# Kernel optimization log

Hardware: AMD Instinct MI355X
Metric: run time of the kernel (lower is better)

Reference implementation:

```python
import jax, jax.numpy as jnp
import numpy as np

N_NODES = 100000
N_EDGES = 1600000
D_IN = 64
D_OUT = 64


def setup_inputs() -> dict:
    key = jax.random.key(0)
    k1, k2, k3, k4, k5 = jax.random.split(key, 5)
    x = jax.random.normal(k1, (N_NODES, D_IN), dtype=jnp.float32)
    edge_src = jax.random.randint(k2, (N_EDGES,), 0, N_NODES, dtype=jnp.int32)
    edge_dst = jax.random.randint(k3, (N_EDGES,), 0, N_NODES, dtype=jnp.int32)
    edge_val = jnp.ones((N_EDGES,), dtype=jnp.float32)
    stdv = 1.0 / np.sqrt(D_OUT)
    weight = jax.random.uniform(k4, (D_IN, D_OUT), minval=-stdv, maxval=stdv, dtype=jnp.float32)
    epsilon = jnp.ones((1,), dtype=jnp.float32)
    bias = jax.random.uniform(k5, (D_OUT,), minval=-stdv, maxval=stdv, dtype=jnp.float32)
    return {"x": x, "edge_src": edge_src, "edge_dst": edge_dst,
            "edge_val": edge_val, "weight": weight, "epsilon": epsilon, "bias": bias}


def reference(x, edge_src, edge_dst, edge_val, weight, epsilon, bias):
    # spmm(adj, x): row i of adj gathers neighbors -> segment_sum over edge_src
    # adj[i, j] = edge_val for edge (src=i, dst=j)
    msgs = edge_val[:, None] * x[edge_dst]            # [E, D_in]
    agg = jax.ops.segment_sum(msgs, edge_src, num_segments=N_NODES)  # [N, D_in]
    # epsilon * eye(N) @ x == epsilon * x (avoid O(N^2) identity)
    rep = agg + epsilon * x                            # [N, D_in]
    out = rep @ weight + bias                          # [N, D_out]
    return out, rep
```

## Files before the change

kernel.cpp:

```cpp
#include <hip/hip_runtime.h>

#define N_NODES 100000
#define N_EDGES 1600000
#define D 64

#define NB 391
#define BLKA 196
#define EPB 8192
#define NT (NB * BLKA)
#define NCH 75

#define WS_GHIST   0
#define WS_PART    76672
#define WS_ROWPTR  76800
#define WS_KEYS    176832
#define WS_PAIRS   1776832

__global__ __launch_bounds__(256) void k_bucket_hist(
    const int* __restrict__ esrc, int* __restrict__ ghist)
{
    __shared__ int h[NB];
    int t = threadIdx.x;
    for (int j = t; j < NB; j += 256) h[j] = 0;
    __syncthreads();
    int base = blockIdx.x * EPB;
    #pragma unroll
    for (int i = 0; i < 8; ++i) {
        int e0 = base + i * 1024 + t * 4;
        if (e0 < N_EDGES) {
            int4 s4 = *(const int4*)(esrc + e0);
            atomicAdd(&h[s4.x >> 8], 1);
            atomicAdd(&h[s4.y >> 8], 1);
            atomicAdd(&h[s4.z >> 8], 1);
            atomicAdd(&h[s4.w >> 8], 1);
        }
    }
    __syncthreads();
    for (int j = t; j < NB; j += 256) ghist[j * BLKA + blockIdx.x] = h[j];
}

__global__ __launch_bounds__(1024) void k_ghist_scan1(
    const int* __restrict__ ghist, int* __restrict__ partial)
{
    __shared__ int sred[16];
    int t = threadIdx.x;
    int idx = blockIdx.x * 1024 + t;
    int v = (idx < NT) ? ghist[idx] : 0;
    #pragma unroll
    for (int off = 32; off; off >>= 1) v += __shfl_down(v, off, 64);
    if ((t & 63) == 0) sred[t >> 6] = v;
    __syncthreads();
    if (t < 16) {
        int w = sred[t];
        #pragma unroll
        for (int off = 8; off; off >>= 1) w += __shfl_down(w, off, 16);
        if (t == 0) partial[blockIdx.x] = w;
    }
}

__global__ __launch_bounds__(1024) void k_ghist_scan2(
    int* __restrict__ ghist, const int* __restrict__ partial)
{
    __shared__ int red1[16];
    __shared__ int wsum[16];
    __shared__ int bc;
    int t = threadIdx.x;
    int lane = t & 63, wid = t >> 6;

    int pv = (t < NCH) ? partial[t] : 0;
    int a1 = (t < (int)blockIdx.x) ? pv : 0;
    #pragma unroll
    for (int off = 32; off; off >>= 1) a1 += __shfl_down(a1, off, 64);
    if (lane == 0) red1[wid] = a1;
    __syncthreads();
    if (t < 16) {
        int w = red1[t];
        #pragma unroll
        for (int off = 8; off; off >>= 1) w += __shfl_down(w, off, 16);
        if (t == 0) bc = w;
    }
    __syncthreads();

    int idx = blockIdx.x * 1024 + t;
    int v = (idx < NT) ? ghist[idx] : 0;
    int s = v;
    #pragma unroll
    for (int off = 1; off < 64; off <<= 1) {
        int y = __shfl_up(s, off, 64);
        if (lane >= off) s += y;
    }
    if (lane == 63) wsum[wid] = s;
    __syncthreads();
    if (t < 16) {
        int w = wsum[t];
        #pragma unroll
        for (int off = 1; off < 16; off <<= 1) {
            int y = __shfl_up(w, off, 16);
            if (t >= off) w += y;
        }
        wsum[t] = w;
    }
    __syncthreads();
    int prefix = wid ? wsum[wid - 1] : 0;
    if (idx < NT) ghist[idx] = bc + prefix + s - v;
}

__global__ __launch_bounds__(256) void k_scatter(
    const int* __restrict__ esrc, const int* __restrict__ edst,
    const float* __restrict__ eval_, const int* __restrict__ ghist,
    int* __restrict__ keys, int2* __restrict__ tpairs)
{
    __shared__ int base[NB];
    int t = threadIdx.x;
    for (int j = t; j < NB; j += 256) base[j] = ghist[j * BLKA + blockIdx.x];
    __syncthreads();
    int eb = blockIdx.x * EPB;
    #pragma unroll
    for (int i = 0; i < 8; ++i) {
        int e0 = eb + i * 1024 + t * 4;
        if (e0 < N_EDGES) {
            int4 s4 = *(const int4*)(esrc + e0);
            int4 d4 = *(const int4*)(edst + e0);
            float4 v4 = *(const float4*)(eval_ + e0);
            int p0 = atomicAdd(&base[s4.x >> 8], 1);
            int p1 = atomicAdd(&base[s4.y >> 8], 1);
            int p2 = atomicAdd(&base[s4.z >> 8], 1);
            int p3 = atomicAdd(&base[s4.w >> 8], 1);
            keys[p0] = s4.x; tpairs[p0] = make_int2(d4.x, __float_as_int(v4.x));
            keys[p1] = s4.y; tpairs[p1] = make_int2(d4.y, __float_as_int(v4.y));
            keys[p2] = s4.z; tpairs[p2] = make_int2(d4.z, __float_as_int(v4.z));
            keys[p3] = s4.w; tpairs[p3] = make_int2(d4.w, __float_as_int(v4.w));
        }
    }
}

__global__ __launch_bounds__(256) void k_build_csr(
    const int* __restrict__ keys, const int2* __restrict__ tpairs,
    const int* __restrict__ ghist, int* __restrict__ row_ptr,
    int2* __restrict__ pairs)
{
    __shared__ int hist[256], cursor[256], wsum4[4];
    int b = blockIdx.x, t = threadIdx.x;
    int s_begin = ghist[b * BLKA];
    int s_end = (b + 1 < NB) ? ghist[(b + 1) * BLKA] : N_EDGES;
    hist[t] = 0;
    __syncthreads();
    #pragma unroll 4
    for (int pos = s_begin + t; pos < s_end; pos += 256)
        atomicAdd(&hist[keys[pos] & 255], 1);
    __syncthreads();
    int lane = t & 63, wid = t >> 6;
    int v = hist[t], s = v;
    #pragma unroll
    for (int off = 1; off < 64; off <<= 1) {
        int y = __shfl_up(s, off, 64);
        if (lane >= off) s += y;
    }
    if (lane == 63) wsum4[wid] = s;
    __syncthreads();
    if (t == 0) {
        int r = 0;
        #pragma unroll
        for (int k = 0; k < 4; ++k) { int x = wsum4[k]; wsum4[k] = r; r += x; }
    }
    __syncthreads();
    int excl = wsum4[wid] + s - v;
    cursor[t] = excl;
    int node = (b << 8) + t;
    if (node <= N_NODES) row_ptr[node] = s_begin + excl;
    __syncthreads();
    #pragma unroll 4
    for (int pos = s_begin + t; pos < s_end; pos += 256) {
        int k = keys[pos] & 255;
        int2 pv = tpairs[pos];
        int p = atomicAdd(&cursor[k], 1);
        pairs[s_begin + p] = pv;
    }
}

#define GATHER_BLOCKS 2048

__global__ __launch_bounds__(256) void k_gather(
    const float* __restrict__ x, const int* __restrict__ row_ptr,
    const int2* __restrict__ pairs, const float* __restrict__ epsilon,
    float* __restrict__ rep)
{
    int w = (blockIdx.x * 256 + threadIdx.x) >> 6;
    int nw = gridDim.x * 4;
    int lane = threadIdx.x & 63;
    int sub = lane >> 4;
    int f4 = lane & 15;
    float eps = epsilon[0];
    const float4* x4 = (const float4*)x;

    int r0 = (int)((long long)w * N_NODES / nw);
    int r1 = (int)((long long)(w + 1) * N_NODES / nw);

    for (int row = r0; row < r1; ++row) {
        int start = __builtin_amdgcn_readfirstlane(row_ptr[row]);
        int end   = __builtin_amdgcn_readfirstlane(row_ptr[row + 1]);
        float4 acc = make_float4(0.f, 0.f, 0.f, 0.f);
        for (int j = start; j < end; j += 16) {
            int2 p[4];
            #pragma unroll
            for (int u = 0; u < 4; ++u) {
                int e = j + u * 4 + sub;
                p[u] = (e < end) ? pairs[e] : make_int2(0, 0);
            }
            float4 a[4];
            #pragma unroll
            for (int u = 0; u < 4; ++u)
                a[u] = x4[(size_t)p[u].x * 16 + f4];
            #pragma unroll
            for (int u = 0; u < 4; ++u) {
                float vv = __int_as_float(p[u].y);
                acc.x += vv * a[u].x; acc.y += vv * a[u].y;
                acc.z += vv * a[u].z; acc.w += vv * a[u].w;
            }
        }
        #pragma unroll
        for (int off = 16; off <= 32; off <<= 1) {
            acc.x += __shfl_xor(acc.x, off, 64);
            acc.y += __shfl_xor(acc.y, off, 64);
            acc.z += __shfl_xor(acc.z, off, 64);
            acc.w += __shfl_xor(acc.w, off, 64);
        }
        if (sub == 0) {
            float4 xv = x4[(size_t)row * 16 + f4];
            float4 o = make_float4(acc.x + eps * xv.x, acc.y + eps * xv.y,
                                   acc.z + eps * xv.z, acc.w + eps * xv.w);
            ((float4*)rep)[(size_t)row * 16 + f4] = o;
        }
    }
}

#define GEMM_TM 64
__global__ __launch_bounds__(256) void k_gemm(
    const float* __restrict__ rep, const float* __restrict__ weight,
    const float* __restrict__ bias, float* __restrict__ out)
{
    __shared__ float rep_s[GEMM_TM * 68];
    __shared__ float Ws[D * D];
    int t = threadIdx.x;
    {
        const float4* w4 = (const float4*)weight;
        float4* s4 = (float4*)Ws;
        #pragma unroll
        for (int i = 0; i < (D * D / 4) / 256; ++i)
            s4[t + i * 256] = w4[t + i * 256];
    }
    int row0 = blockIdx.x * GEMM_TM;
    {
        const float4* r4 = (const float4*)rep;
        #pragma unroll
        for (int i = 0; i < 4; ++i) {
            int f = t + i * 256;
            int rr = f >> 4, kk4 = f & 15;
            float4 v = (row0 + rr < N_NODES) ? r4[(size_t)(row0 + rr) * 16 + kk4]
                                             : make_float4(0.f, 0.f, 0.f, 0.f);
            rep_s[rr * 68 + kk4 * 4 + 0] = v.x;
            rep_s[rr * 68 + kk4 * 4 + 1] = v.y;
            rep_s[rr * 68 + kk4 * 4 + 2] = v.z;
            rep_s[rr * 68 + kk4 * 4 + 3] = v.w;
        }
    }
    __syncthreads();

    int tx = t & 15, ty = t >> 4;
    float4 b4 = ((const float4*)bias)[tx];
    float acc[4][4];
    #pragma unroll
    for (int i = 0; i < 4; ++i) {
        acc[i][0] = b4.x; acc[i][1] = b4.y; acc[i][2] = b4.z; acc[i][3] = b4.w;
    }
    #pragma unroll 4
    for (int k4 = 0; k4 < 16; ++k4) {
        float4 rv[4];
        #pragma unroll
        for (int i = 0; i < 4; ++i)
            rv[i] = *(const float4*)&rep_s[(ty * 4 + i) * 68 + k4 * 4];
        #pragma unroll
        for (int kk = 0; kk < 4; ++kk) {
            float4 wv = *(const float4*)&Ws[(k4 * 4 + kk) * D + tx * 4];
            #pragma unroll
            for (int i = 0; i < 4; ++i) {
                float r = ((const float*)&rv[i])[kk];
                acc[i][0] += r * wv.x;
                acc[i][1] += r * wv.y;
                acc[i][2] += r * wv.z;
                acc[i][3] += r * wv.w;
            }
        }
    }
    #pragma unroll
    for (int i = 0; i < 4; ++i) {
        int row = row0 + ty * 4 + i;
        if (row < N_NODES)
            *(float4*)&out[(size_t)row * D + tx * 4] =
                make_float4(acc[i][0], acc[i][1], acc[i][2], acc[i][3]);
    }
}

extern "C" void kernel_launch(void* const* d_in, const int* in_sizes, int n_in,
                              void* d_out, int out_size, void* d_ws, size_t ws_size,
                              hipStream_t stream) {
    const float* x    = (const float*)d_in[0];
    const int*   esrc = (const int*)  d_in[1];
    const int*   edst = (const int*)  d_in[2];
    const float* ev   = (const float*)d_in[3];
    const float* w    = (const float*)d_in[4];
    const float* eps  = (const float*)d_in[5];
    const float* bias = (const float*)d_in[6];

    float* out = (float*)d_out;
    float* rep = out + (size_t)N_NODES * D;

    int* ws      = (int*)d_ws;
    int* ghist   = ws + WS_GHIST;
    int* partial = ws + WS_PART;
    int* row_ptr = ws + WS_ROWPTR;
    int* keys    = ws + WS_KEYS;
    int2* pairs  = (int2*)(ws + WS_PAIRS);
    int2* tpairs = (int2*)rep;

    k_bucket_hist<<<BLKA, 256, 0, stream>>>(esrc, ghist);
    k_ghist_scan1<<<NCH, 1024, 0, stream>>>(ghist, partial);
    k_ghist_scan2<<<NCH, 1024, 0, stream>>>(ghist, partial);
    k_scatter<<<BLKA, 256, 0, stream>>>(esrc, edst, ev, ghist, keys, tpairs);
    k_build_csr<<<NB, 256, 0, stream>>>(keys, tpairs, ghist, row_ptr, pairs);
    k_gather<<<GATHER_BLOCKS, 256, 0, stream>>>(x, row_ptr, pairs, eps, rep);
    k_gemm<<<(N_NODES + GEMM_TM - 1) / GEMM_TM, 256, 0, stream>>>(rep, w, bias, out);
}
```

Before: 236.5 us.

## Replace full CSR build with 64-node bucket sort and shared-memory atomic accumulation

Buckets edges by 64-node tiles instead of 256-node buckets, drops the second-level CSR build kernel, and packs the local row index into the pair's high bits. A new per-tile gather kernel accumulates messages into a shared-memory tile with LDS float atomics, using rotated columns to spread bank conflicts, then adds eps*x and writes rep. This removes one full pass over the edge list and the keys array, at the cost of LDS atomic contention, scalar 4-byte x loads instead of float4, and a larger bucket histogram and scan.

```diff
diff --git a/kernel.cpp b/kernel.cpp
--- a/kernel.cpp
+++ b/kernel.cpp
@@ -4,24 +4,23 @@
 #define N_EDGES 1600000
 #define D 64
 
-#define NB 391
+#define TILE_N 64
+#define NBUK 1563
 #define BLKA 196
 #define EPB 8192
-#define NT (NB * BLKA)
-#define NCH 75
+#define NT (NBUK * BLKA)
+#define NCH 300
 
 #define WS_GHIST   0
-#define WS_PART    76672
-#define WS_ROWPTR  76800
-#define WS_KEYS    176832
-#define WS_PAIRS   1776832
+#define WS_PART    306432
+#define WS_TPAIRS  306816
 
 __global__ __launch_bounds__(256) void k_bucket_hist(
     const int* __restrict__ esrc, int* __restrict__ ghist)
 {
-    __shared__ int h[NB];
-    int t = threadIdx.x;
-    for (int j = t; j < NB; j += 256) h[j] = 0;
+    __shared__ int h[NBUK];
+    int t = threadIdx.x;
+    for (int j = t; j < NBUK; j += 256) h[j] = 0;
     __syncthreads();
     int base = blockIdx.x * EPB;
     #pragma unroll
@@ -29,14 +28,14 @@
         int e0 = base + i * 1024 + t * 4;
         if (e0 < N_EDGES) {
             int4 s4 = *(const int4*)(esrc + e0);
-            atomicAdd(&h[s4.x >> 8], 1);
-            atomicAdd(&h[s4.y >> 8], 1);
-            atomicAdd(&h[s4.z >> 8], 1);
-            atomicAdd(&h[s4.w >> 8], 1);
-        }
-    }
-    __syncthreads();
-    for (int j = t; j < NB; j += 256) ghist[j * BLKA + blockIdx.x] = h[j];
+            atomicAdd(&h[s4.x >> 6], 1);
+            atomicAdd(&h[s4.y >> 6], 1);
+            atomicAdd(&h[s4.z >> 6], 1);
+            atomicAdd(&h[s4.w >> 6], 1);
+        }
+    }
+    __syncthreads();
+    for (int j = t; j < NBUK; j += 256) ghist[j * BLKA + blockIdx.x] = h[j];
 }
 
 __global__ __launch_bounds__(1024) void k_ghist_scan1(
@@ -108,11 +107,11 @@
 __global__ __launch_bounds__(256) void k_scatter(
     const int* __restrict__ esrc, const int* __restrict__ edst,
     const float* __restrict__ eval_, const int* __restrict__ ghist,
-    int* __restrict__ keys, int2* __restrict__ tpairs)
-{
-    __shared__ int base[NB];
-    int t = threadIdx.x;
-    for (int j = t; j < NB; j += 256) base[j] = ghist[j * BLKA + blockIdx.x];
+    int2* __restrict__ tpairs)
+{
+    __shared__ int base[NBUK];
+    int t = threadIdx.x;
+    for (int j = t; j < NBUK; j += 256) base[j] = ghist[j * BLKA + blockIdx.x];
     __syncthreads();
     int eb = blockIdx.x * EPB;
     #pragma unroll
@@ -122,114 +121,84 @@
             int4 s4 = *(const int4*)(esrc + e0);
             int4 d4 = *(const int4*)(edst + e0);
             float4 v4 = *(const float4*)(eval_ + e0);
-            int p0 = atomicAdd(&base[s4.x >> 8], 1);
-            int p1 = atomicAdd(&base[s4.y >> 8], 1);
-            int p2 = atomicAdd(&base[s4.z >> 8], 1);
-            int p3 = atomicAdd(&base[s4.w >> 8], 1);
-            keys[p0] = s4.x; tpairs[p0] = make_int2(d4.x, __float_as_int(v4.x));
-            keys[p1] = s4.y; tpairs[p1] = make_int2(d4.y, __float_as_int(v4.y));
-            keys[p2] = s4.z; tpairs[p2] = make_int2(d4.z, __float_as_int(v4.z));
-            keys[p3] = s4.w; tpairs[p3] = make_int2(d4.w, __float_as_int(v4.w));
-        }
-    }
-}
-
-__global__ __launch_bounds__(256) void k_build_csr(
-    const int* __restrict__ keys, const int2* __restrict__ tpairs,
-    const int* __restrict__ ghist, int* __restrict__ row_ptr,
-    int2* __restrict__ pairs)
-{
-    __shared__ int hist[256], cursor[256], wsum4[4];
+            int p0 = atomicAdd(&base[s4.x >> 6], 1);
+            int p1 = atomicAdd(&base[s4.y >> 6], 1);
+            int p2 = atomicAdd(&base[s4.z >> 6], 1);
+            int p3 = atomicAdd(&base[s4.w >> 6], 1);
+            tpairs[p0] = make_int2(((s4.x & 63) << 17) | d4.x, __float_as_int(v4.x));
+            tpairs[p1] = make_int2(((s4.y & 63) << 17) | d4.y, __float_as_int(v4.y));
+            tpairs[p2] = make_int2(((s4.z & 63) << 17) | d4.z, __float_as_int(v4.z));
+            tpairs[p3] = make_int2(((s4.w & 63) << 17) | d4.w, __float_as_int(v4.w));
+        }
+    }
+}
+
+__global__ __launch_bounds__(256) void k_tile_gather(
+    const float* __restrict__ x, const int2* __restrict__ tpairs,
+    const int* __restrict__ ghist, const float* __restrict__ epsilon,
+    float* __restrict__ rep)
+{
+    __shared__ float tile[TILE_N * D];
     int b = blockIdx.x, t = threadIdx.x;
-    int s_begin = ghist[b * BLKA];
-    int s_end = (b + 1 < NB) ? ghist[(b + 1) * BLKA] : N_EDGES;
-    hist[t] = 0;
-    __syncthreads();
-    #pragma unroll 4
-    for (int pos = s_begin + t; pos < s_end; pos += 256)
-        atomicAdd(&hist[keys[pos] & 255], 1);
-    __syncthreads();
-    int lane = t & 63, wid = t >> 6;
-    int v = hist[t], s = v;
-    #pragma unroll
-    for (int off = 1; off < 64; off <<= 1) {
-        int y = __shfl_up(s, off, 64);
-        if (lane >= off) s += y;
-    }
-    if (lane == 63) wsum4[wid] = s;
-    __syncthreads();
-    if (t == 0) {
-        int r = 0;
-        #pragma unroll
-        for (int k = 0; k < 4; ++k) { int x = wsum4[k]; wsum4[k] = r; r += x; }
-    }
-    __syncthreads();
-    int excl = wsum4[wid] + s - v;
-    cursor[t] = excl;
-    int node = (b << 8) + t;
-    if (node <= N_NODES) row_ptr[node] = s_begin + excl;
-    __syncthreads();
-    #pragma unroll 4
-    for (int pos = s_begin + t; pos < s_end; pos += 256) {
-        int k = keys[pos] & 255;
-        int2 pv = tpairs[pos];
-        int p = atomicAdd(&cursor[k], 1);
-        pairs[s_begin + p] = pv;
-    }
-}
-
-#define GATHER_BLOCKS 2048
-
-__global__ __launch_bounds__(256) void k_gather(
-    const float* __restrict__ x, const int* __restrict__ row_ptr,
-    const int2* __restrict__ pairs, const float* __restrict__ epsilon,
-    float* __restrict__ rep)
-{
-    int w = (blockIdx.x * 256 + threadIdx.x) >> 6;
-    int nw = gridDim.x * 4;
-    int lane = threadIdx.x & 63;
-    int sub = lane >> 4;
-    int f4 = lane & 15;
+    {
+        float4* t4 = (float4*)tile;
+        #pragma unroll
+        for (int i = 0; i < 4; ++i)
+            t4[t + i * 256] = make_float4(0.f, 0.f, 0.f, 0.f);
+    }
+    __syncthreads();
+
+    int begin = ghist[b * BLKA];
+    int end   = (b + 1 < NBUK) ? ghist[(b + 1) * BLKA] : N_EDGES;
+
+    int wv = t >> 6, lane = t & 63;
+    int sub = lane >> 4, f4 = lane & 15;
+
+    for (int j = begin + wv * 16; j < end; j += 4 * 16) {
+        int2 p[4];
+        #pragma unroll
+        for (int u = 0; u < 4; ++u) {
+            int e = j + u * 4 + sub;
+            p[u] = (e < end) ? tpairs[e] : make_int2(0, 0);
+        }
+        float a[4][4];
+        #pragma unroll
+        for (int u = 0; u < 4; ++u) {
+            int dst = p[u].x & 0x1FFFF;
+            #pragma unroll
+            for (int c = 0; c < 4; ++c)
+                a[u][c] = x[dst * D + f4 + 16 * c];
+        }
+        #pragma unroll
+        for (int u = 0; u < 4; ++u) {
+            float vv = __int_as_float(p[u].y);
+            int n = p[u].x >> 17;
+            #pragma unroll
+            for (int c = 0; c < 4; ++c) {
+                int col = (f4 + 16 * c + n) & 63;
+                atomicAdd(&tile[n * D + col], vv * a[u][c]);
+            }
+        }
+    }
+    __syncthreads();
+
     float eps = epsilon[0];
+    int n0 = b * TILE_N;
     const float4* x4 = (const float4*)x;
-
-    int r0 = (int)((long long)w * N_NODES / nw);
-    int r1 = (int)((long long)(w + 1) * N_NODES / nw);
-
-    for (int row = r0; row < r1; ++row) {
-        int start = __builtin_amdgcn_readfirstlane(row_ptr[row]);
-        int end   = __builtin_amdgcn_readfirstlane(row_ptr[row + 1]);
-        float4 acc = make_float4(0.f, 0.f, 0.f, 0.f);
-        for (int j = start; j < end; j += 16) {
-            int2 p[4];
-            #pragma unroll
-            for (int u = 0; u < 4; ++u) {
-                int e = j + u * 4 + sub;
-                p[u] = (e < end) ? pairs[e] : make_int2(0, 0);
-            }
-            float4 a[4];
-            #pragma unroll
-            for (int u = 0; u < 4; ++u)
-                a[u] = x4[(size_t)p[u].x * 16 + f4];
-            #pragma unroll
-            for (int u = 0; u < 4; ++u) {
-                float vv = __int_as_float(p[u].y);
-                acc.x += vv * a[u].x; acc.y += vv * a[u].y;
-                acc.z += vv * a[u].z; acc.w += vv * a[u].w;
-            }
-        }
-        #pragma unroll
-        for (int off = 16; off <= 32; off <<= 1) {
-            acc.x += __shfl_xor(acc.x, off, 64);
-            acc.y += __shfl_xor(acc.y, off, 64);
-            acc.z += __shfl_xor(acc.z, off, 64);
-            acc.w += __shfl_xor(acc.w, off, 64);
-        }
-        if (sub == 0) {
-            float4 xv = x4[(size_t)row * 16 + f4];
-            float4 o = make_float4(acc.x + eps * xv.x, acc.y + eps * xv.y,
-                                   acc.z + eps * xv.z, acc.w + eps * xv.w);
-            ((float4*)rep)[(size_t)row * 16 + f4] = o;
+    #pragma unroll
+    for (int i = 0; i < 4; ++i) {
+        int f = t + i * 256;
+        int n = f >> 4, c4 = f & 15;
+        int node = n0 + n;
+        if (node < N_NODES) {
+            float r0 = tile[n * D + ((c4 * 4 + 0 + n) & 63)];
+            float r1 = tile[n * D + ((c4 * 4 + 1 + n) & 63)];
+            float r2 = tile[n * D + ((c4 * 4 + 2 + n) & 63)];
+            float r3 = tile[n * D + ((c4 * 4 + 3 + n) & 63)];
+            float4 xv = x4[(size_t)node * 16 + c4];
+            ((float4*)rep)[(size_t)node * 16 + c4] =
+                make_float4(r0 + eps * xv.x, r1 + eps * xv.y,
+                            r2 + eps * xv.z, r3 + eps * xv.w);
         }
     }
 }
@@ -318,16 +287,12 @@
     int* ws      = (int*)d_ws;
     int* ghist   = ws + WS_GHIST;
     int* partial = ws + WS_PART;
-    int* row_ptr = ws + WS_ROWPTR;
-    int* keys    = ws + WS_KEYS;
-    int2* pairs  = (int2*)(ws + WS_PAIRS);
-    int2* tpairs = (int2*)rep;
+    int2* tpairs = (int2*)(ws + WS_TPAIRS);
 
     k_bucket_hist<<<BLKA, 256, 0, stream>>>(esrc, ghist);
     k_ghist_scan1<<<NCH, 1024, 0, stream>>>(ghist, partial);
     k_ghist_scan2<<<NCH, 1024, 0, stream>>>(ghist, partial);
-    k_scatter<<<BLKA, 256, 0, stream>>>(esrc, edst, ev, ghist, keys, tpairs);
-    k_build_csr<<<NB, 256, 0, stream>>>(keys, tpairs, ghist, row_ptr, pairs);
-    k_gather<<<GATHER_BLOCKS, 256, 0, stream>>>(x, row_ptr, pairs, eps, rep);
+    k_scatter<<<BLKA, 256, 0, stream>>>(esrc, edst, ev, ghist, tpairs);
+    k_tile_gather<<<NBUK, 256, 0, stream>>>(x, tpairs, ghist, eps, rep);
     k_gemm<<<(N_NODES + GEMM_TM - 1) / GEMM_TM, 256, 0, stream>>>(rep, w, bias, out);
 }
```

New measurement: 739.3 us. +212.6%, slower.

## Pack low source bits into pair word, drop keys array, use finer buckets

Applied to the files above, without the earlier changes.

The separate keys array is removed. The low 7 bits of each source node are packed into the upper bits of the destination index inside the pair (dst fits in 17 bits), and the gather masks them off. Buckets shrink from 256 to 128 nodes and blocks shrink to 2048 edges, giving 782 buckets and 782 histogram blocks. This cuts a 1.6M-element write and read. In exchange the global histogram grows to about 611K entries and the scan gets more blocks.

```diff
diff --git a/kernel.cpp b/kernel.cpp
--- a/kernel.cpp
+++ b/kernel.cpp
@@ -4,19 +4,18 @@
 #define N_EDGES 1600000
 #define D 64
 
-#define NB 391
-#define BLKA 196
-#define EPB 8192
+#define NB 782
+#define BLKA 782
+#define EPB 2048
 #define NT (NB * BLKA)
-#define NCH 75
+#define NCH 598
 
 #define WS_GHIST   0
-#define WS_PART    76672
-#define WS_ROWPTR  76800
-#define WS_KEYS    176832
-#define WS_PAIRS   1776832
-
-__global__ __launch_bounds__(256) void k_bucket_hist(
+#define WS_PART    611584
+#define WS_ROWPTR  612224
+#define WS_PAIRS   712256
+
+__global__ __launch_bounds__(256) void k_hist(
     const int* __restrict__ esrc, int* __restrict__ ghist)
 {
     __shared__ int h[NB];
@@ -25,21 +24,21 @@
     __syncthreads();
     int base = blockIdx.x * EPB;
     #pragma unroll
-    for (int i = 0; i < 8; ++i) {
+    for (int i = 0; i < 2; ++i) {
         int e0 = base + i * 1024 + t * 4;
         if (e0 < N_EDGES) {
             int4 s4 = *(const int4*)(esrc + e0);
-            atomicAdd(&h[s4.x >> 8], 1);
-            atomicAdd(&h[s4.y >> 8], 1);
-            atomicAdd(&h[s4.z >> 8], 1);
-            atomicAdd(&h[s4.w >> 8], 1);
+            atomicAdd(&h[s4.x >> 7], 1);
+            atomicAdd(&h[s4.y >> 7], 1);
+            atomicAdd(&h[s4.z >> 7], 1);
+            atomicAdd(&h[s4.w >> 7], 1);
         }
     }
     __syncthreads();
     for (int j = t; j < NB; j += 256) ghist[j * BLKA + blockIdx.x] = h[j];
 }
 
-__global__ __launch_bounds__(1024) void k_ghist_scan1(
+__global__ __launch_bounds__(1024) void k_scan1(
     const int* __restrict__ ghist, int* __restrict__ partial)
 {
     __shared__ int sred[16];
@@ -58,7 +57,7 @@
     }
 }
 
-__global__ __launch_bounds__(1024) void k_ghist_scan2(
+__global__ __launch_bounds__(1024) void k_scan2(
     int* __restrict__ ghist, const int* __restrict__ partial)
 {
     __shared__ int red1[16];
@@ -108,7 +107,7 @@
 __global__ __launch_bounds__(256) void k_scatter(
     const int* __restrict__ esrc, const int* __restrict__ edst,
     const float* __restrict__ eval_, const int* __restrict__ ghist,
-    int* __restrict__ keys, int2* __restrict__ tpairs)
+    int2* __restrict__ tpairs)
 {
     __shared__ int base[NB];
     int t = threadIdx.x;
@@ -116,63 +115,63 @@
     __syncthreads();
     int eb = blockIdx.x * EPB;
     #pragma unroll
-    for (int i = 0; i < 8; ++i) {
+    for (int i = 0; i < 2; ++i) {
         int e0 = eb + i * 1024 + t * 4;
         if (e0 < N_EDGES) {
             int4 s4 = *(const int4*)(esrc + e0);
             int4 d4 = *(const int4*)(edst + e0);
             float4 v4 = *(const float4*)(eval_ + e0);
-            int p0 = atomicAdd(&base[s4.x >> 8], 1);
-            int p1 = atomicAdd(&base[s4.y >> 8], 1);
-            int p2 = atomicAdd(&base[s4.z >> 8], 1);
-            int p3 = atomicAdd(&base[s4.w >> 8], 1);
-            keys[p0] = s4.x; tpairs[p0] = make_int2(d4.x, __float_as_int(v4.x));
-            keys[p1] = s4.y; tpairs[p1] = make_int2(d4.y, __float_as_int(v4.y));
-            keys[p2] = s4.z; tpairs[p2] = make_int2(d4.z, __float_as_int(v4.z));
-            keys[p3] = s4.w; tpairs[p3] = make_int2(d4.w, __float_as_int(v4.w));
-        }
-    }
-}
-
-__global__ __launch_bounds__(256) void k_build_csr(
-    const int* __restrict__ keys, const int2* __restrict__ tpairs,
-    const int* __restrict__ ghist, int* __restrict__ row_ptr,
-    int2* __restrict__ pairs)
-{
-    __shared__ int hist[256], cursor[256], wsum4[4];
+            int p0 = atomicAdd(&base[s4.x >> 7], 1);
+            int p1 = atomicAdd(&base[s4.y >> 7], 1);
+            int p2 = atomicAdd(&base[s4.z >> 7], 1);
+            int p3 = atomicAdd(&base[s4.w >> 7], 1);
+            tpairs[p0] = make_int2(((s4.x & 127) << 17) | d4.x, __float_as_int(v4.x));
+            tpairs[p1] = make_int2(((s4.y & 127) << 17) | d4.y, __float_as_int(v4.y));
+            tpairs[p2] = make_int2(((s4.z & 127) << 17) | d4.z, __float_as_int(v4.z));
+            tpairs[p3] = make_int2(((s4.w & 127) << 17) | d4.w, __float_as_int(v4.w));
+        }
+    }
+}
+
+__global__ __launch_bounds__(256) void k_build(
+    const int2* __restrict__ tpairs, const int* __restrict__ ghist,
+    int* __restrict__ row_ptr, int2* __restrict__ pairs)
+{
+    __shared__ int hist[128], cursor[128], wsum2[2];
     int b = blockIdx.x, t = threadIdx.x;
     int s_begin = ghist[b * BLKA];
     int s_end = (b + 1 < NB) ? ghist[(b + 1) * BLKA] : N_EDGES;
-    hist[t] = 0;
+    if (t < 128) hist[t] = 0;
     __syncthreads();
     #pragma unroll 4
     for (int pos = s_begin + t; pos < s_end; pos += 256)
-        atomicAdd(&hist[keys[pos] & 255], 1);
+        atomicAdd(&hist[(tpairs[pos].x >> 17) & 127], 1);
     __syncthreads();
     int lane = t & 63, wid = t >> 6;
-    int v = hist[t], s = v;
-    #pragma unroll
-    for (int off = 1; off < 64; off <<= 1) {
-        int y = __shfl_up(s, off, 64);
-        if (lane >= off) s += y;
-    }
-    if (lane == 63) wsum4[wid] = s;
-    __syncthreads();
-    if (t == 0) {
-        int r = 0;
-        #pragma unroll
-        for (int k = 0; k < 4; ++k) { int x = wsum4[k]; wsum4[k] = r; r += x; }
-    }
-    __syncthreads();
-    int excl = wsum4[wid] + s - v;
-    cursor[t] = excl;
-    int node = (b << 8) + t;
-    if (node <= N_NODES) row_ptr[node] = s_begin + excl;
+    int v = 0, s = 0;
+    if (t < 128) {
+        v = hist[t]; s = v;
+        #pragma unroll
+        for (int off = 1; off < 64; off <<= 1) {
+            int y = __shfl_up(s, off, 64);
+            if (lane >= off) s += y;
+        }
+        if (lane == 63) wsum2[wid] = s;
+    }
+    __syncthreads();
+    if (t == 0) { int x0 = wsum2[0]; wsum2[0] = 0; wsum2[1] = x0; }
+    __syncthreads();
+    if (t < 128) {
+        int excl = wsum2[wid] + s - v;
+        cursor[t] = excl;
+        int node = (b << 7) + t;
+        if (node <= N_NODES) row_ptr[node] = s_begin + excl;
+    }
     __syncthreads();
     #pragma unroll 4
     for (int pos = s_begin + t; pos < s_end; pos += 256) {
-        int k = keys[pos] & 255;
         int2 pv = tpairs[pos];
+        int k = (pv.x >> 17) & 127;
         int p = atomicAdd(&cursor[k], 1);
         pairs[s_begin + p] = pv;
     }
@@ -210,7 +209,7 @@
             float4 a[4];
             #pragma unroll
             for (int u = 0; u < 4; ++u)
-                a[u] = x4[(size_t)p[u].x * 16 + f4];
+                a[u] = x4[(size_t)(p[u].x & 0x1FFFF) * 16 + f4];
             #pragma unroll
             for (int u = 0; u < 4; ++u) {
                 float vv = __int_as_float(p[u].y);
@@ -319,15 +318,14 @@
     int* ghist   = ws + WS_GHIST;
     int* partial = ws + WS_PART;
     int* row_ptr = ws + WS_ROWPTR;
-    int* keys    = ws + WS_KEYS;
     int2* pairs  = (int2*)(ws + WS_PAIRS);
     int2* tpairs = (int2*)rep;
 
-    k_bucket_hist<<<BLKA, 256, 0, stream>>>(esrc, ghist);
-    k_ghist_scan1<<<NCH, 1024, 0, stream>>>(ghist, partial);
-    k_ghist_scan2<<<NCH, 1024, 0, stream>>>(ghist, partial);
-    k_scatter<<<BLKA, 256, 0, stream>>>(esrc, edst, ev, ghist, keys, tpairs);
-    k_build_csr<<<NB, 256, 0, stream>>>(keys, tpairs, ghist, row_ptr, pairs);
+    k_hist<<<BLKA, 256, 0, stream>>>(esrc, ghist);
+    k_scan1<<<NCH, 1024, 0, stream>>>(ghist, partial);
+    k_scan2<<<NCH, 1024, 0, stream>>>(ghist, partial);
+    k_scatter<<<BLKA, 256, 0, stream>>>(esrc, edst, ev, ghist, tpairs);
+    k_build<<<NB, 256, 0, stream>>>(tpairs, ghist, row_ptr, pairs);
     k_gather<<<GATHER_BLOCKS, 256, 0, stream>>>(x, row_ptr, pairs, eps, rep);
     k_gemm<<<(N_NODES + GEMM_TM - 1) / GEMM_TM, 256, 0, stream>>>(rep, w, bias, out);
 }
```

After: 222.5 us. -5.9%, faster.

## Gather from fp16 copy of x and pack edges into 32-bit words

Applied to the files above, without the earlier changes.

Converts x to fp16 in the histogram kernel and has the gather read half-precision rows, which halves the random-gather traffic. The separate keys array is dropped by packing the low source bits into the destination field. CSR entries shrink to 32 bits: 17 bits of destination plus a 15-bit truncated half of the edge value. The cost is precision loss in both x and the edge weights (the value drops its lowest mantissa bit), which could break tolerance for general inputs. The bucketing grid is also doubled to 391 blocks of 4096 edges.

```diff
diff --git a/kernel.cpp b/kernel.cpp
--- a/kernel.cpp
+++ b/kernel.cpp
@@ -1,23 +1,25 @@
 #include <hip/hip_runtime.h>
+#include <hip/hip_fp16.h>
 
 #define N_NODES 100000
 #define N_EDGES 1600000
 #define D 64
 
 #define NB 391
-#define BLKA 196
-#define EPB 8192
+#define BLKA 391
+#define EPB 4096
 #define NT (NB * BLKA)
-#define NCH 75
+#define NCH 150
 
 #define WS_GHIST   0
-#define WS_PART    76672
-#define WS_ROWPTR  76800
-#define WS_KEYS    176832
-#define WS_PAIRS   1776832
-
-__global__ __launch_bounds__(256) void k_bucket_hist(
-    const int* __restrict__ esrc, int* __restrict__ ghist)
+#define WS_PART    152896
+#define WS_ROWPTR  153152
+#define WS_PAIRSU  253184
+#define WS_XH      1853184
+
+__global__ __launch_bounds__(256) void k_hist_cvt(
+    const int* __restrict__ esrc, const float* __restrict__ x,
+    int* __restrict__ ghist, uint2* __restrict__ xh2)
 {
     __shared__ int h[NB];
     int t = threadIdx.x;
@@ -25,7 +27,7 @@
     __syncthreads();
     int base = blockIdx.x * EPB;
     #pragma unroll
-    for (int i = 0; i < 8; ++i) {
+    for (int i = 0; i < 4; ++i) {
         int e0 = base + i * 1024 + t * 4;
         if (e0 < N_EDGES) {
             int4 s4 = *(const int4*)(esrc + e0);
@@ -35,11 +37,27 @@
             atomicAdd(&h[s4.w >> 8], 1);
         }
     }
+    {
+        const float4* x4 = (const float4*)x;
+        #pragma unroll
+        for (int i = 0; i < 16; ++i) {
+            int f = blockIdx.x * 4096 + i * 256 + t;
+            if (f < N_NODES * (D / 4)) {
+                float4 v = x4[f];
+                uint2 o;
+                o.x = (uint)__half_as_ushort(__float2half_rn(v.x)) |
+                      ((uint)__half_as_ushort(__float2half_rn(v.y)) << 16);
+                o.y = (uint)__half_as_ushort(__float2half_rn(v.z)) |
+                      ((uint)__half_as_ushort(__float2half_rn(v.w)) << 16);
+                xh2[f] = o;
+            }
+        }
+    }
     __syncthreads();
     for (int j = t; j < NB; j += 256) ghist[j * BLKA + blockIdx.x] = h[j];
 }
 
-__global__ __launch_bounds__(1024) void k_ghist_scan1(
+__global__ __launch_bounds__(1024) void k_scan1(
     const int* __restrict__ ghist, int* __restrict__ partial)
 {
     __shared__ int sred[16];
@@ -58,7 +76,7 @@
     }
 }
 
-__global__ __launch_bounds__(1024) void k_ghist_scan2(
+__global__ __launch_bounds__(1024) void k_scan2(
     int* __restrict__ ghist, const int* __restrict__ partial)
 {
     __shared__ int red1[16];
@@ -108,7 +126,7 @@
 __global__ __launch_bounds__(256) void k_scatter(
     const int* __restrict__ esrc, const int* __restrict__ edst,
     const float* __restrict__ eval_, const int* __restrict__ ghist,
-    int* __restrict__ keys, int2* __restrict__ tpairs)
+    int2* __restrict__ tpairs)
 {
     __shared__ int base[NB];
     int t = threadIdx.x;
@@ -116,7 +134,7 @@
     __syncthreads();
     int eb = blockIdx.x * EPB;
     #pragma unroll
-    for (int i = 0; i < 8; ++i) {
+    for (int i = 0; i < 4; ++i) {
         int e0 = eb + i * 1024 + t * 4;
         if (e0 < N_EDGES) {
             int4 s4 = *(const int4*)(esrc + e0);
@@ -126,18 +144,17 @@
             int p1 = atomicAdd(&base[s4.y >> 8], 1);
             int p2 = atomicAdd(&base[s4.z >> 8], 1);
             int p3 = atomicAdd(&base[s4.w >> 8], 1);
-            keys[p0] = s4.x; tpairs[p0] = make_int2(d4.x, __float_as_int(v4.x));
-            keys[p1] = s4.y; tpairs[p1] = make_int2(d4.y, __float_as_int(v4.y));
-            keys[p2] = s4.z; tpairs[p2] = make_int2(d4.z, __float_as_int(v4.z));
-            keys[p3] = s4.w; tpairs[p3] = make_int2(d4.w, __float_as_int(v4.w));
-        }
-    }
-}
-
-__global__ __launch_bounds__(256) void k_build_csr(
-    const int* __restrict__ keys, const int2* __restrict__ tpairs,
-    const int* __restrict__ ghist, int* __restrict__ row_ptr,
-    int2* __restrict__ pairs)
+            tpairs[p0] = make_int2(((s4.x & 255) << 17) | d4.x, __float_as_int(v4.x));
+            tpairs[p1] = make_int2(((s4.y & 255) << 17) | d4.y, __float_as_int(v4.y));
+            tpairs[p2] = make_int2(((s4.z & 255) << 17) | d4.z, __float_as_int(v4.z));
+            tpairs[p3] = make_int2(((s4.w & 255) << 17) | d4.w, __float_as_int(v4.w));
+        }
+    }
+}
+
+__global__ __launch_bounds__(256) void k_build(
+    const int2* __restrict__ tpairs, const int* __restrict__ ghist,
+    int* __restrict__ row_ptr, unsigned int* __restrict__ pairsu)
 {
     __shared__ int hist[256], cursor[256], wsum4[4];
     int b = blockIdx.x, t = threadIdx.x;
@@ -147,7 +164,7 @@
     __syncthreads();
     #pragma unroll 4
     for (int pos = s_begin + t; pos < s_end; pos += 256)
-        atomicAdd(&hist[keys[pos] & 255], 1);
+        atomicAdd(&hist[(tpairs[pos].x >> 17) & 255], 1);
     __syncthreads();
     int lane = t & 63, wid = t >> 6;
     int v = hist[t], s = v;
@@ -161,7 +178,7 @@
     if (t == 0) {
         int r = 0;
         #pragma unroll
-        for (int k = 0; k < 4; ++k) { int x = wsum4[k]; wsum4[k] = r; r += x; }
+        for (int k = 0; k < 4; ++k) { int w = wsum4[k]; wsum4[k] = r; r += w; }
     }
     __syncthreads();
     int excl = wsum4[wid] + s - v;
@@ -171,19 +188,22 @@
     __syncthreads();
     #pragma unroll 4
     for (int pos = s_begin + t; pos < s_end; pos += 256) {
-        int k = keys[pos] & 255;
         int2 pv = tpairs[pos];
+        int k = (pv.x >> 17) & 255;
         int p = atomicAdd(&cursor[k], 1);
-        pairs[s_begin + p] = pv;
+        unsigned int dst = (unsigned int)pv.x & 0x1FFFFu;
+        unsigned int hb = (unsigned int)__half_as_ushort(
+            __float2half_rn(__int_as_float(pv.y)));
+        pairsu[s_begin + p] = (dst << 15) | (hb >> 1);
     }
 }
 
 #define GATHER_BLOCKS 2048
 
 __global__ __launch_bounds__(256) void k_gather(
-    const float* __restrict__ x, const int* __restrict__ row_ptr,
-    const int2* __restrict__ pairs, const float* __restrict__ epsilon,
-    float* __restrict__ rep)
+    const float* __restrict__ x, const uint2* __restrict__ xh2,
+    const int* __restrict__ row_ptr, const unsigned int* __restrict__ pairsu,
+    const float* __restrict__ epsilon, float* __restrict__ rep)
 {
     int w = (blockIdx.x * 256 + threadIdx.x) >> 6;
     int nw = gridDim.x * 4;
@@ -201,21 +221,24 @@
         int end   = __builtin_amdgcn_readfirstlane(row_ptr[row + 1]);
         float4 acc = make_float4(0.f, 0.f, 0.f, 0.f);
         for (int j = start; j < end; j += 16) {
-            int2 p[4];
+            unsigned int pk[4];
             #pragma unroll
             for (int u = 0; u < 4; ++u) {
                 int e = j + u * 4 + sub;
-                p[u] = (e < end) ? pairs[e] : make_int2(0, 0);
+                pk[u] = (e < end) ? pairsu[e] : 0u;
             }
-            float4 a[4];
+            uint2 a[4];
             #pragma unroll
             for (int u = 0; u < 4; ++u)
-                a[u] = x4[(size_t)p[u].x * 16 + f4];
+                a[u] = xh2[(size_t)(pk[u] >> 15) * 16 + f4];
             #pragma unroll
             for (int u = 0; u < 4; ++u) {
-                float vv = __int_as_float(p[u].y);
-                acc.x += vv * a[u].x; acc.y += vv * a[u].y;
-                acc.z += vv * a[u].z; acc.w += vv * a[u].w;
+                unsigned short hb = (unsigned short)((pk[u] & 0x7FFFu) << 1);
+                float vv = __half2float(__ushort_as_half(hb));
+                float2 f01 = __half22float2(*reinterpret_cast<const __half2*>(&a[u].x));
+                float2 f23 = __half22float2(*reinterpret_cast<const __half2*>(&a[u].y));
+                acc.x += vv * f01.x; acc.y += vv * f01.y;
+                acc.z += vv * f23.x; acc.w += vv * f23.y;
             }
         }
         #pragma unroll
@@ -315,19 +338,19 @@
     float* out = (float*)d_out;
     float* rep = out + (size_t)N_NODES * D;
 
-    int* ws      = (int*)d_ws;
-    int* ghist   = ws + WS_GHIST;
-    int* partial = ws + WS_PART;
-    int* row_ptr = ws + WS_ROWPTR;
-    int* keys    = ws + WS_KEYS;
-    int2* pairs  = (int2*)(ws + WS_PAIRS);
-    int2* tpairs = (int2*)rep;
-
-    k_bucket_hist<<<BLKA, 256, 0, stream>>>(esrc, ghist);
-    k_ghist_scan1<<<NCH, 1024, 0, stream>>>(ghist, partial);
-    k_ghist_scan2<<<NCH, 1024, 0, stream>>>(ghist, partial);
-    k_scatter<<<BLKA, 256, 0, stream>>>(esrc, edst, ev, ghist, keys, tpairs);
-    k_build_csr<<<NB, 256, 0, stream>>>(keys, tpairs, ghist, row_ptr, pairs);
-    k_gather<<<GATHER_BLOCKS, 256, 0, stream>>>(x, row_ptr, pairs, eps, rep);
+    int* ws       = (int*)d_ws;
+    int* ghist    = ws + WS_GHIST;
+    int* partial  = ws + WS_PART;
+    int* row_ptr  = ws + WS_ROWPTR;
+    unsigned int* pairsu = (unsigned int*)(ws + WS_PAIRSU);
+    uint2* xh2    = (uint2*)(ws + WS_XH);
+    int2* tpairs  = (int2*)rep;
+
+    k_hist_cvt<<<BLKA, 256, 0, stream>>>(esrc, x, ghist, xh2);
+    k_scan1<<<NCH, 1024, 0, stream>>>(ghist, partial);
+    k_scan2<<<NCH, 1024, 0, stream>>>(ghist, partial);
+    k_scatter<<<BLKA, 256, 0, stream>>>(esrc, edst, ev, ghist, tpairs);
+    k_build<<<NB, 256, 0, stream>>>(tpairs, ghist, row_ptr, pairsu);
+    k_gather<<<GATHER_BLOCKS, 256, 0, stream>>>(x, xh2, row_ptr, pairsu, eps, rep);
     k_gemm<<<(N_NODES + GEMM_TM - 1) / GEMM_TM, 256, 0, stream>>>(rep, w, bias, out);
 }
```

Result: faster. 199.9 us (-15.5%).
